# Optimization experiments

Hardware: AMD Instinct MI355X
Metric: run time of the kernel (lower is better)

The kernel has to match this reference:

```python
import jax, jax.numpy as jnp
import numpy as np

B, K, T, C = 4, 8, 2048, 64

def setup_inputs() -> dict:
    key = jax.random.key(0)
    ks = jax.random.split(key, 7)
    return {
        "x": jax.random.normal(ks[0], (B, K, T, C), dtype=jnp.float32),
        "Wq": jax.random.normal(ks[1], (C, C), dtype=jnp.float32) / np.sqrt(C),
        "bq": jax.random.normal(ks[2], (C,), dtype=jnp.float32) * 0.01,
        "Wk": jax.random.normal(ks[3], (C, C), dtype=jnp.float32) / np.sqrt(C),
        "bk": jax.random.normal(ks[4], (C,), dtype=jnp.float32) * 0.01,
        "Wv": jax.random.normal(ks[5], (C, C), dtype=jnp.float32) / np.sqrt(C),
        "bv": jax.random.normal(ks[6], (C,), dtype=jnp.float32) * 0.01,
    }

def reference(x, Wq, bq, Wk, bk, Wv, bv):
    c_dim = x.shape[-1]
    # torch nn.Linear: y = x @ W.T + b
    q = jnp.einsum('bktc,dc->bktd', x, Wq) + bq
    k = jnp.einsum('bktc,dc->bktd', x, Wk) + bk
    v = jnp.einsum('bktc,dc->bktd', x, Wv) + bv
    scores = jnp.einsum('bkic,bkjc->bkij', q, k) / jnp.sqrt(jnp.float32(c_dim))
    attn = jax.nn.softmax(scores, axis=-1)
    out = jnp.einsum('bkij,bkjc->bkic', attn, v)
    return out
```

## Files before the change

kernel.cpp:

```cpp
#include <hip/hip_runtime.h>


#define T_DIM 2048
#define NHEAD 32
#define HSTRIDE (T_DIM * 64)
#define QSCALE 0.18033688011112042f
#define SOFF  8.0f

#define SWZ(row, grp) ((row) * 64 + ((((grp) ^ ((row) & 7)) & 7) * 8))

typedef _Float16 h8 __attribute__((ext_vector_type(8)));
typedef _Float16 h4 __attribute__((ext_vector_type(4)));
typedef __fp16   g2 __attribute__((ext_vector_type(2)));
typedef float    f4 __attribute__((ext_vector_type(4)));
typedef float    fv16 __attribute__((ext_vector_type(16)));

union H4U { h4 v; g2 p[2]; };
union H8U { h8 v; h4 h[2]; g2 p[4]; };

#if defined(__has_builtin)
#if __has_builtin(__builtin_amdgcn_exp2f)
#define EXP2(x) __builtin_amdgcn_exp2f(x)
#endif
#endif
#ifndef EXP2
__device__ inline float exp2_raw(float x) {
    float r;
    asm("v_exp_f32 %0, %1" : "=v"(r) : "v"(x));
    return r;
}
#define EXP2(x) exp2_raw(x)
#endif

__device__ inline h4 cvt4(f4 x) {
    H4U u;
    u.p[0] = __builtin_amdgcn_cvt_pkrtz(x[0], x[1]);
    u.p[1] = __builtin_amdgcn_cvt_pkrtz(x[2], x[3]);
    return u.v;
}

__device__ inline h8 cvt8(f4 a, f4 b) {
    H8U r;
    r.h[0] = cvt4(a);
    r.h[1] = cvt4(b);
    return r.v;
}

__device__ inline fv16 splat16(float x) {
    fv16 r;
    #pragma unroll
    for (int i = 0; i < 16; ++i) r[i] = x;
    return r;
}

__global__ __launch_bounds__(256) void qkv_proj_kernel(
    const float* __restrict__ x,
    const float* __restrict__ Wq, const float* __restrict__ bq,
    const float* __restrict__ Wk, const float* __restrict__ bk,
    const float* __restrict__ Wv, const float* __restrict__ bv,
    _Float16* __restrict__ qh, _Float16* __restrict__ khT,
    _Float16* __restrict__ vtT)
{
    __shared__ _Float16 ws[3][64 * 64];
    __shared__ float bsh[3][64];

    const int tid  = threadIdx.x;
    const int row0 = blockIdx.x * 64;
    const int head = blockIdx.x >> 5;
    const int t0   = (blockIdx.x & 31) * 64;

    const int w    = tid >> 6;
    const int lane = tid & 63;
    const int l15  = lane & 15;
    const int qd   = lane >> 4;

    f4 xa[2][2];
    {
        const float* xp = x + (size_t)(row0 + w * 16 + l15) * 64 + qd * 8;
        #pragma unroll
        for (int ch = 0; ch < 2; ++ch) {
            xa[ch][0] = *(const f4*)(xp + ch * 32);
            xa[ch][1] = *(const f4*)(xp + ch * 32 + 4);
        }
    }

    #pragma unroll
    for (int m = 0; m < 3; ++m) {
        const float* Wm = (m == 0) ? Wq : ((m == 1) ? Wk : Wv);
        const float* bm = (m == 0) ? bq : ((m == 1) ? bk : bv);
        #pragma unroll
        for (int pass = 0; pass < 4; ++pass) {
            const int idx = pass * 1024 + tid * 4;
            const int d = idx >> 6, c = idx & 63;
            f4 wv = *(const f4*)(Wm + idx);
            *(h4*)&ws[m][SWZ(d, c >> 3) + (c & 7)] = cvt4(wv);
        }
        if (tid < 64) bsh[m][tid] = bm[tid];
    }

    h8 af[2];
    #pragma unroll
    for (int ch = 0; ch < 2; ++ch)
        af[ch] = cvt8(xa[ch][0], xa[ch][1]);

    __syncthreads();

    f4 acc[3][4];
    #pragma unroll
    for (int m = 0; m < 3; ++m) {
        h8 bf[4][2];
        #pragma unroll
        for (int ns = 0; ns < 4; ++ns)
            #pragma unroll
            for (int ch = 0; ch < 2; ++ch)
                bf[ns][ch] = *(const h8*)&ws[m][SWZ(ns * 16 + l15, ch * 4 + qd)];
        #pragma unroll
        for (int ns = 0; ns < 4; ++ns)
            acc[m][ns] = (f4){0.f, 0.f, 0.f, 0.f};
        #pragma unroll
        for (int ch = 0; ch < 2; ++ch)
            #pragma unroll
            for (int ns = 0; ns < 4; ++ns)
                acc[m][ns] = __builtin_amdgcn_mfma_f32_16x16x32_f16(
                    af[ch], bf[ns][ch], acc[m][ns], 0, 0, 0);
    }

    __syncthreads();

    #pragma unroll
    for (int m = 0; m < 2; ++m) {
        #pragma unroll
        for (int ns = 0; ns < 4; ++ns) {
            const int d = ns * 16 + l15;
            const float bias = bsh[m][d];
            #pragma unroll
            for (int r = 0; r < 4; ++r) {
                const int t = w * 16 + qd * 4 + r;
                float v = acc[m][ns][r] + bias;
                if (m == 0) v *= QSCALE;
                ws[m][SWZ(t, d >> 3) + (d & 7)] = (_Float16)v;
            }
        }
    }
    #pragma unroll
    for (int ns = 0; ns < 4; ++ns) {
        const int d = ns * 16 + l15;
        const float bias = bsh[2][d];
        const int tl = w * 16 + qd * 4;
        f4 pvf;
        #pragma unroll
        for (int r = 0; r < 4; ++r)
            pvf[r] = acc[2][ns][r] + bias;
        *(h4*)&ws[2][SWZ(d, tl >> 3) + (tl & 7)] = cvt4(pvf);
    }

    __syncthreads();

    #pragma unroll
    for (int pass = 0; pass < 2; ++pass) {
        const int t  = pass * 32 + (tid >> 3);
        const int c0 = (tid & 7) * 8;
        *(h8*)&qh[(size_t)(row0 + t) * 64 + c0] =
            *(const h8*)&ws[0][SWZ(t, tid & 7)];
    }
    #pragma unroll
    for (int pass = 0; pass < 2; ++pass) {
        const int f   = pass * 2048 + tid * 8;
        const int kb  = f >> 11;
        const int cs  = (f >> 9) & 3;
        const int l   = (f >> 3) & 63;
        const int p   = l & 31;
        const int w16 = p & 15;
        const int sw  = ((w16 & 12) == 4) ? (w16 + 4)
                      : (((w16 & 12) == 8) ? (w16 - 4) : w16);
        const int tact = kb * 32 + (p & 16) + sw;
        const int g8   = cs * 2 + (l >> 5);
        *(h8*)&khT[(size_t)head * HSTRIDE + (t0 >> 6) * 4096 + f] =
            *(const h8*)&ws[1][SWZ(tact, g8)];
    }
    #pragma unroll
    for (int pass = 0; pass < 2; ++pass) {
        const int f  = pass * 2048 + tid * 8;
        const int q2 = f >> 9;
        const int b  = q2 >> 1, cc = q2 & 1;
        const int l  = (f >> 3) & 63;
        const int c  = cc * 32 + (l & 31);
        const int tg = b * 2 + (l >> 5);
        *(h8*)&vtT[(size_t)head * HSTRIDE + (t0 >> 6) * 4096 + f] =
            *(const h8*)&ws[2][SWZ(c, tg)];
    }
}

__global__ __launch_bounds__(256, 2) void attn_kernel(
    const _Float16* __restrict__ qh, const _Float16* __restrict__ khT,
    const _Float16* __restrict__ vtT, float* __restrict__ out)
{
    __shared__ float xbuf[4][2304];

    const int tid  = threadIdx.x;
    const int w    = tid >> 6;
    const int lane = tid & 63;
    const int l31  = lane & 31;
    const int lh   = lane >> 5;
    const int qg   = w >> 1;
    const int ph   = w & 1;

    const int bid  = blockIdx.x;
    const int xcd  = bid & 7;
    const int slot = bid >> 3;
    const int head = xcd * 4 + (slot >> 4);
    const int qpart = slot & 15;
    const int q0   = qpart * 128 + qg * 64;

    h8 qf[2][4];
    #pragma unroll
    for (int qs = 0; qs < 2; ++qs) {
        const _Float16* qp = qh + (size_t)(head * T_DIM + q0 + qs * 32 + l31) * 64 + lh * 8;
        #pragma unroll
        for (int cs = 0; cs < 4; ++cs)
            qf[qs][cs] = *(const h8*)(qp + cs * 16);
    }

    const int ko = lane * 8;
    const _Float16* kbase = khT + (size_t)head * HSTRIDE + (size_t)ph * 16 * 4096;
    const _Float16* vbase = vtT + (size_t)head * HSTRIDE + (size_t)ph * 16 * 4096;

    f4 rs4[2] = {(f4){0.f,0.f,0.f,0.f}, (f4){0.f,0.f,0.f,0.f}};
    fv16 oacc[2][2];
    #pragma unroll
    for (int qs = 0; qs < 2; ++qs)
        #pragma unroll
        for (int cc = 0; cc < 2; ++cc)
            oacc[qs][cc] = splat16(0.f);

    h8 kf[2][4];
    h8 vf[4][2];
    #pragma unroll
    for (int kb = 0; kb < 2; ++kb)
        #pragma unroll
        for (int cs = 0; cs < 4; ++cs)
            kf[kb][cs] = *(const h8*)(kbase + kb * 2048 + cs * 512 + ko);
    #pragma unroll
    for (int b = 0; b < 4; ++b)
        #pragma unroll
        for (int cc = 0; cc < 2; ++cc)
            vf[b][cc] = *(const h8*)(vbase + (b * 2 + cc) * 512 + ko);

    for (int it = 0; it < 16; ++it) {
        const _Float16* kn = kbase + (size_t)(it + 1) * 4096;
        const _Float16* vn = vbase + (size_t)(it + 1) * 4096;
        const bool more = (it < 15);

        #pragma unroll
        for (int kb = 0; kb < 2; ++kb) {
            fv16 st2[2];
            st2[0] = splat16(-SOFF);
            st2[1] = splat16(-SOFF);
            #pragma unroll
            for (int cs = 0; cs < 4; ++cs)
                #pragma unroll
                for (int qs = 0; qs < 2; ++qs)
                    st2[qs] = __builtin_amdgcn_mfma_f32_32x32x16_f16(
                        kf[kb][cs], qf[qs][cs], st2[qs], 0, 0, 0);

            if (more) {
                #pragma unroll
                for (int cs = 0; cs < 4; ++cs)
                    kf[kb][cs] = *(const h8*)(kn + kb * 2048 + cs * 512 + ko);
            }

            #pragma unroll
            for (int qs = 0; qs < 2; ++qs) {
                f4 pg[4];
                #pragma unroll
                for (int g = 0; g < 4; ++g) {
                    pg[g][0] = EXP2(st2[qs][4 * g + 0]);
                    pg[g][1] = EXP2(st2[qs][4 * g + 1]);
                    pg[g][2] = EXP2(st2[qs][4 * g + 2]);
                    pg[g][3] = EXP2(st2[qs][4 * g + 3]);
                    rs4[qs] += pg[g];
                }
                H8U pa[2];
                #pragma unroll
                for (int g = 0; g < 4; ++g) {
                    pa[g >> 1].p[(g & 1) * 2 + 0] = __builtin_amdgcn_cvt_pkrtz(pg[g][0], pg[g][1]);
                    pa[g >> 1].p[(g & 1) * 2 + 1] = __builtin_amdgcn_cvt_pkrtz(pg[g][2], pg[g][3]);
                }
                #pragma unroll
                for (int bl = 0; bl < 2; ++bl)
                    #pragma unroll
                    for (int cc = 0; cc < 2; ++cc)
                        oacc[qs][cc] = __builtin_amdgcn_mfma_f32_32x32x16_f16(
                            pa[bl].v, vf[kb * 2 + bl][cc], oacc[qs][cc], 0, 0, 0);
            }

            if (more) {
                #pragma unroll
                for (int bl = 0; bl < 2; ++bl)
                    #pragma unroll
                    for (int cc = 0; cc < 2; ++cc)
                        vf[kb * 2 + bl][cc] =
                            *(const h8*)(vn + ((kb * 2 + bl) * 2 + cc) * 512 + ko);
            }
        }
    }

    {
        float* xb = xbuf[w];
        if (ph == 0) {
            #pragma unroll
            for (int cc = 0; cc < 2; ++cc)
                #pragma unroll
                for (int r = 0; r < 16; ++r)
                    xb[(cc * 16 + r) * 64 + lane] = oacc[1][cc][r];
            #pragma unroll
            for (int i = 0; i < 4; ++i)
                xb[2048 + i * 64 + lane] = rs4[1][i];
        } else {
            #pragma unroll
            for (int cc = 0; cc < 2; ++cc)
                #pragma unroll
                for (int r = 0; r < 16; ++r)
                    xb[(cc * 16 + r) * 64 + lane] = oacc[0][cc][r];
            #pragma unroll
            for (int i = 0; i < 4; ++i)
                xb[2048 + i * 64 + lane] = rs4[0][i];
        }
    }

    __syncthreads();

    const float* pb = xbuf[w ^ 1];
    fv16 of[2];
    f4 rsf;
    if (ph == 0) {
        #pragma unroll
        for (int cc = 0; cc < 2; ++cc)
            #pragma unroll
            for (int r = 0; r < 16; ++r)
                of[cc][r] = oacc[0][cc][r] + pb[(cc * 16 + r) * 64 + lane];
        #pragma unroll
        for (int i = 0; i < 4; ++i)
            rsf[i] = rs4[0][i] + pb[2048 + i * 64 + lane];
    } else {
        #pragma unroll
        for (int cc = 0; cc < 2; ++cc)
            #pragma unroll
            for (int r = 0; r < 16; ++r)
                of[cc][r] = oacc[1][cc][r] + pb[(cc * 16 + r) * 64 + lane];
        #pragma unroll
        for (int i = 0; i < 4; ++i)
            rsf[i] = rs4[1][i] + pb[2048 + i * 64 + lane];
    }

    float lsum = (rsf[0] + rsf[1]) + (rsf[2] + rsf[3]);
    lsum += __shfl_xor(lsum, 32, 64);
    const float linv = 1.f / lsum;
    #pragma unroll
    for (int r = 0; r < 16; ++r) {
        const int qrow = (r & 3) + 8 * (r >> 2) + 4 * lh;
        const float fac = __shfl(linv, qrow, 64);
        #pragma unroll
        for (int cc = 0; cc < 2; ++cc)
            out[(size_t)(head * T_DIM + q0 + ph * 32 + qrow) * 64 + cc * 32 + l31] =
                of[cc][r] * fac;
    }
}

extern "C" void kernel_launch(void* const* d_in, const int* in_sizes, int n_in,
                              void* d_out, int out_size, void* d_ws, size_t ws_size,
                              hipStream_t stream)
{
    (void)in_sizes; (void)n_in; (void)out_size; (void)ws_size;
    const float* x  = (const float*)d_in[0];
    const float* Wq = (const float*)d_in[1];
    const float* bq = (const float*)d_in[2];
    const float* Wk = (const float*)d_in[3];
    const float* bk = (const float*)d_in[4];
    const float* Wv = (const float*)d_in[5];
    const float* bv = (const float*)d_in[6];
    float* out = (float*)d_out;

    _Float16* qh  = (_Float16*)d_ws;
    _Float16* khT = qh + (size_t)NHEAD * HSTRIDE;
    _Float16* vtT = khT + (size_t)NHEAD * HSTRIDE;

    hipLaunchKernelGGL(qkv_proj_kernel, dim3(1024), dim3(256), 0, stream,
                       x, Wq, bq, Wk, bk, Wv, bv, qh, khT, vtT);
    hipLaunchKernelGGL(attn_kernel, dim3(512), dim3(256), 0, stream,
                       qh, khT, vtT, out);
}
```

Measured before the change: 123.6 us.

## Software-pipeline QK^T one tile ahead of softmax/PV in attention loop

Restructures the attention main loop so the QK^T scores for the next K tile are computed while the exp2 and PV MFMAs of the current tile run. K fragments are now prefetched two iterations ahead, and V fragments are loaded just in time at the start of each half-iteration instead of being kept in registers a full iteration ahead. The goal is to overlap MFMA work with transcendental work and hide K load latency. Launch bounds drop to one block per CU occupancy hint, which allows more registers for the extra score accumulators but may reduce latency hiding from occupancy, and V loads are now exposed closer to their use.

```diff
diff --git a/kernel.cpp b/kernel.cpp
--- a/kernel.cpp
+++ b/kernel.cpp
@@ -191,7 +191,7 @@
     }
 }
 
-__global__ __launch_bounds__(256, 2) void attn_kernel(
+__global__ __launch_bounds__(256, 1) void attn_kernel(
     const _Float16* __restrict__ qh, const _Float16* __restrict__ khT,
     const _Float16* __restrict__ vtT, float* __restrict__ out)
 {
@@ -234,51 +234,64 @@
             oacc[qs][cc] = splat16(0.f);
 
     h8 kf[2][4];
-    h8 vf[4][2];
     #pragma unroll
     for (int kb = 0; kb < 2; ++kb)
         #pragma unroll
         for (int cs = 0; cs < 4; ++cs)
             kf[kb][cs] = *(const h8*)(kbase + kb * 2048 + cs * 512 + ko);
-    #pragma unroll
-    for (int b = 0; b < 4; ++b)
-        #pragma unroll
-        for (int cc = 0; cc < 2; ++cc)
-            vf[b][cc] = *(const h8*)(vbase + (b * 2 + cc) * 512 + ko);
+
+    fv16 stA[2], stB[2];
+    stA[0] = splat16(-SOFF); stA[1] = splat16(-SOFF);
+    stB[0] = splat16(-SOFF); stB[1] = splat16(-SOFF);
+    #pragma unroll
+    for (int cs = 0; cs < 4; ++cs)
+        #pragma unroll
+        for (int qs = 0; qs < 2; ++qs) {
+            stA[qs] = __builtin_amdgcn_mfma_f32_32x32x16_f16(
+                kf[0][cs], qf[qs][cs], stA[qs], 0, 0, 0);
+            stB[qs] = __builtin_amdgcn_mfma_f32_32x32x16_f16(
+                kf[1][cs], qf[qs][cs], stB[qs], 0, 0, 0);
+        }
+    {
+        const _Float16* kn1 = kbase + 4096;
+        #pragma unroll
+        for (int kb = 0; kb < 2; ++kb)
+            #pragma unroll
+            for (int cs = 0; cs < 4; ++cs)
+                kf[kb][cs] = *(const h8*)(kn1 + kb * 2048 + cs * 512 + ko);
+    }
 
     for (int it = 0; it < 16; ++it) {
-        const _Float16* kn = kbase + (size_t)(it + 1) * 4096;
-        const _Float16* vn = vbase + (size_t)(it + 1) * 4096;
-        const bool more = (it < 15);
-
-        #pragma unroll
-        for (int kb = 0; kb < 2; ++kb) {
-            fv16 st2[2];
-            st2[0] = splat16(-SOFF);
-            st2[1] = splat16(-SOFF);
-            #pragma unroll
-            for (int cs = 0; cs < 4; ++cs)
-                #pragma unroll
-                for (int qs = 0; qs < 2; ++qs)
-                    st2[qs] = __builtin_amdgcn_mfma_f32_32x32x16_f16(
-                        kf[kb][cs], qf[qs][cs], st2[qs], 0, 0, 0);
-
-            if (more) {
-                #pragma unroll
-                for (int cs = 0; cs < 4; ++cs)
-                    kf[kb][cs] = *(const h8*)(kn + kb * 2048 + cs * 512 + ko);
-            }
+        const bool more  = (it < 15);
+        const bool more2 = (it < 14);
+        const _Float16* vcur = vbase + (size_t)it * 4096;
+        const _Float16* kn2  = kbase + (size_t)(it + 2) * 4096;
+
+        {
+            h8 vf0[2][2];
+            #pragma unroll
+            for (int bl = 0; bl < 2; ++bl)
+                #pragma unroll
+                for (int cc = 0; cc < 2; ++cc)
+                    vf0[bl][cc] = *(const h8*)(vcur + (bl * 2 + cc) * 512 + ko);
 
             #pragma unroll
             for (int qs = 0; qs < 2; ++qs) {
                 f4 pg[4];
                 #pragma unroll
                 for (int g = 0; g < 4; ++g) {
-                    pg[g][0] = EXP2(st2[qs][4 * g + 0]);
-                    pg[g][1] = EXP2(st2[qs][4 * g + 1]);
-                    pg[g][2] = EXP2(st2[qs][4 * g + 2]);
-                    pg[g][3] = EXP2(st2[qs][4 * g + 3]);
+                    pg[g][0] = EXP2(stA[qs][4 * g + 0]);
+                    pg[g][1] = EXP2(stA[qs][4 * g + 1]);
+                    pg[g][2] = EXP2(stA[qs][4 * g + 2]);
+                    pg[g][3] = EXP2(stA[qs][4 * g + 3]);
                     rs4[qs] += pg[g];
+                }
+                if (more) {
+                    stA[qs] = splat16(-SOFF);
+                    #pragma unroll
+                    for (int cs = 0; cs < 4; ++cs)
+                        stA[qs] = __builtin_amdgcn_mfma_f32_32x32x16_f16(
+                            kf[0][cs], qf[qs][cs], stA[qs], 0, 0, 0);
                 }
                 H8U pa[2];
                 #pragma unroll
@@ -291,16 +304,58 @@
                     #pragma unroll
                     for (int cc = 0; cc < 2; ++cc)
                         oacc[qs][cc] = __builtin_amdgcn_mfma_f32_32x32x16_f16(
-                            pa[bl].v, vf[kb * 2 + bl][cc], oacc[qs][cc], 0, 0, 0);
+                            pa[bl].v, vf0[bl][cc], oacc[qs][cc], 0, 0, 0);
             }
-
-            if (more) {
+            if (more2) {
+                #pragma unroll
+                for (int cs = 0; cs < 4; ++cs)
+                    kf[0][cs] = *(const h8*)(kn2 + cs * 512 + ko);
+            }
+        }
+
+        {
+            h8 vf1[2][2];
+            #pragma unroll
+            for (int bl = 0; bl < 2; ++bl)
+                #pragma unroll
+                for (int cc = 0; cc < 2; ++cc)
+                    vf1[bl][cc] = *(const h8*)(vcur + ((2 + bl) * 2 + cc) * 512 + ko);
+
+            #pragma unroll
+            for (int qs = 0; qs < 2; ++qs) {
+                f4 pg[4];
+                #pragma unroll
+                for (int g = 0; g < 4; ++g) {
+                    pg[g][0] = EXP2(stB[qs][4 * g + 0]);
+                    pg[g][1] = EXP2(stB[qs][4 * g + 1]);
+                    pg[g][2] = EXP2(stB[qs][4 * g + 2]);
+                    pg[g][3] = EXP2(stB[qs][4 * g + 3]);
+                    rs4[qs] += pg[g];
+                }
+                if (more) {
+                    stB[qs] = splat16(-SOFF);
+                    #pragma unroll
+                    for (int cs = 0; cs < 4; ++cs)
+                        stB[qs] = __builtin_amdgcn_mfma_f32_32x32x16_f16(
+                            kf[1][cs], qf[qs][cs], stB[qs], 0, 0, 0);
+                }
+                H8U pa[2];
+                #pragma unroll
+                for (int g = 0; g < 4; ++g) {
+                    pa[g >> 1].p[(g & 1) * 2 + 0] = __builtin_amdgcn_cvt_pkrtz(pg[g][0], pg[g][1]);
+                    pa[g >> 1].p[(g & 1) * 2 + 1] = __builtin_amdgcn_cvt_pkrtz(pg[g][2], pg[g][3]);
+                }
                 #pragma unroll
                 for (int bl = 0; bl < 2; ++bl)
                     #pragma unroll
                     for (int cc = 0; cc < 2; ++cc)
-                        vf[kb * 2 + bl][cc] =
-                            *(const h8*)(vn + ((kb * 2 + bl) * 2 + cc) * 512 + ko);
+                        oacc[qs][cc] = __builtin_amdgcn_mfma_f32_32x32x16_f16(
+                            pa[bl].v, vf1[bl][cc], oacc[qs][cc], 0, 0, 0);
+            }
+            if (more2) {
+                #pragma unroll
+                for (int cs = 0; cs < 4; ++cs)
+                    kf[1][cs] = *(const h8*)(kn2 + 2048 + cs * 512 + ko);
             }
         }
     }
```

Result: no change. 125.2 us (+1.3%).
